# Kernel tuning notes

Measured on AMD Instinct MI355X. Metric: run time of the kernel, lower is better.

Reference implementation:

```python
import jax, jax.numpy as jnp
import numpy as np

N_NODES = 80000


def gcn_conv(x, W, b, src, dst, n_nodes):
    """PyG GCNConv: add self-loops, symmetric normalization, linear, scatter-add, bias."""
    h = x @ W  # [N, out]
    loop = jnp.arange(n_nodes, dtype=src.dtype)
    s = jnp.concatenate([src, loop])  # [E+N]
    d = jnp.concatenate([dst, loop])
    deg = jax.ops.segment_sum(jnp.ones_like(d, dtype=h.dtype), d, num_segments=n_nodes)
    dinv = jnp.where(deg > 0, jax.lax.rsqrt(deg), 0.0)  # deg^-0.5, inf->0
    norm = dinv[s] * dinv[d]  # [E+N]
    msg = h[s] * norm[:, None]  # gather + scale
    out = jax.ops.segment_sum(msg, d, num_segments=n_nodes)  # scatter-add at dst
    return out + b


def setup_inputs() -> dict:
    key = jax.random.key(0)
    ks = jax.random.split(key, 8)
    n_in, n_hid, n_out = 64, 64, 32
    n_edges = 1280000
    x = jax.random.normal(ks[0], (N_NODES, n_in), dtype=jnp.float32)
    edge_index = jax.random.randint(ks[1], (2, n_edges), 0, N_NODES, dtype=jnp.int64)
    def glorot(k, fan_in, fan_out):
        lim = np.sqrt(6.0 / (fan_in + fan_out))
        return jax.random.uniform(k, (fan_in, fan_out), jnp.float32, -lim, lim)
    return {
        "x": x,
        "W1": glorot(ks[2], n_in, n_hid), "b1": jnp.zeros((n_hid,), jnp.float32),
        "W2": glorot(ks[3], n_hid, n_hid), "b2": jnp.zeros((n_hid,), jnp.float32),
        "W3": glorot(ks[4], n_hid, n_out), "b3": jnp.zeros((n_out,), jnp.float32),
        "edge_index": edge_index,
    }


def reference(x, W1, b1, W2, b2, W3, b3, edge_index):
    src, dst = edge_index[0], edge_index[1]
    n = x.shape[0]
    # eval mode: dropout(p=0.2) is identity
    h = jax.nn.elu(gcn_conv(x, W1, b1, src, dst, n))
    h = jax.nn.elu(gcn_conv(h, W2, b2, src, dst, n))
    return gcn_conv(h, W3, b3, src, dst, n)
```

## Files before the change

kernel.cpp:

```cpp
#include <hip/hip_runtime.h>
#include <cmath>


__global__ __launch_bounds__(256) void k_hist_gemm1(
    const int* __restrict__ dst, int nE, int nN,
    int* __restrict__ cnt4, int* __restrict__ rankp,
    const float* __restrict__ x, const float* __restrict__ W,
    float* __restrict__ h, int n) {
    constexpr int OUT = 64;
    constexpr int CG = OUT / 4;
    constexpr int RG = 256 / CG;
    constexpr int ROWS = RG * 4;
    constexpr int XLD = 68;
    __shared__ float Ws[64 * OUT];
    __shared__ float xs[ROWS * XLD];

    const int tid = threadIdx.x;

    if (blockIdx.x & 1) {
        const int bid = blockIdx.x >> 1;
        const int t = bid * 256 + tid;
        const int e0 = t * 4;
        const int sh = (tid >> 6) & 3;
        int* __restrict__ mycnt = cnt4 + (size_t)sh * nN;
        if (e0 + 4 <= nE) {
            int4 d = *reinterpret_cast<const int4*>(dst + e0);
            int r0 = atomicAdd(&mycnt[d.x], 1);
            int r1 = atomicAdd(&mycnt[d.y], 1);
            int r2 = atomicAdd(&mycnt[d.z], 1);
            int r3 = atomicAdd(&mycnt[d.w], 1);
            *reinterpret_cast<int4*>(rankp + e0) =
                make_int4(r0 | (sh << 28), r1 | (sh << 28),
                          r2 | (sh << 28), r3 | (sh << 28));
        } else {
            for (int e = e0; e < nE; ++e)
                rankp[e] = atomicAdd(&mycnt[dst[e]], 1) | (sh << 28);
        }
        return;
    }

    const int bid = blockIdx.x >> 1;
    const int row0 = bid * ROWS;

#pragma unroll
    for (int i = tid * 4; i < 64 * OUT; i += 1024)
        *reinterpret_cast<float4*>(&Ws[i]) =
            *reinterpret_cast<const float4*>(&W[i]);

#pragma unroll
    for (int it = 0; it < ROWS / 16; ++it) {
        const int flat = it * 1024 + tid * 4;
        const int r = flat >> 6;
        const int k = flat & 63;
        float4 v;
        if (row0 + r < n)
            v = *reinterpret_cast<const float4*>(x + (size_t)(row0 + r) * 64 + k);
        else
            v = make_float4(0.f, 0.f, 0.f, 0.f);
        *reinterpret_cast<float4*>(&xs[r * XLD + k]) = v;
    }
    __syncthreads();

    const int rg = tid / CG;
    const int cg = tid % CG;
    const int r0 = rg * 4;

    float4 acc[4];
#pragma unroll
    for (int i = 0; i < 4; ++i) acc[i] = make_float4(0.f, 0.f, 0.f, 0.f);

#pragma unroll 2
    for (int kc = 0; kc < 16; ++kc) {
        float4 xr[4], wk[4];
#pragma unroll
        for (int i = 0; i < 4; ++i)
            xr[i] = *reinterpret_cast<const float4*>(&xs[(r0 + i) * XLD + kc * 4]);
#pragma unroll
        for (int kk = 0; kk < 4; ++kk)
            wk[kk] = *reinterpret_cast<const float4*>(&Ws[(kc * 4 + kk) * OUT + cg * 4]);
#pragma unroll
        for (int kk = 0; kk < 4; ++kk) {
#pragma unroll
            for (int i = 0; i < 4; ++i) {
                const float xv = (kk == 0) ? xr[i].x
                               : (kk == 1) ? xr[i].y
                               : (kk == 2) ? xr[i].z
                                           : xr[i].w;
                acc[i].x += xv * wk[kk].x;
                acc[i].y += xv * wk[kk].y;
                acc[i].z += xv * wk[kk].z;
                acc[i].w += xv * wk[kk].w;
            }
        }
    }

#pragma unroll
    for (int i = 0; i < 4; ++i) {
        const int row = row0 + r0 + i;
        if (row < n)
            *reinterpret_cast<float4*>(h + (size_t)row * OUT + cg * 4) = acc[i];
    }
}

__global__ __launch_bounds__(256) void k_scan1(const int* __restrict__ cnt4, int n,
                                               int* __restrict__ bsum) {
    __shared__ int s[256];
    int i = blockIdx.x * 256 + threadIdx.x;
    int v = 0;
    if (i < n)
        v = cnt4[i] + cnt4[n + i] + cnt4[2 * n + i] + cnt4[3 * n + i];
    s[threadIdx.x] = v;
    __syncthreads();
    for (int off = 128; off > 0; off >>= 1) {
        if (threadIdx.x < off) s[threadIdx.x] += s[threadIdx.x + off];
        __syncthreads();
    }
    if (threadIdx.x == 0) bsum[blockIdx.x] = s[0];
}

__global__ __launch_bounds__(256) void k_scan3(const int* __restrict__ cnt4, int n,
                                               const int* __restrict__ bsum,
                                               int* __restrict__ row_start,
                                               int4* __restrict__ base4,
                                               float* __restrict__ dinv) {
    __shared__ int red[256];
    __shared__ int s[256];
    const int bid = blockIdx.x;
    int part = 0;
    for (int i = threadIdx.x; i < bid; i += 256) part += bsum[i];
    red[threadIdx.x] = part;
    __syncthreads();
    for (int off = 128; off > 0; off >>= 1) {
        if (threadIdx.x < off) red[threadIdx.x] += red[threadIdx.x + off];
        __syncthreads();
    }
    const int boff = red[0];

    int i = bid * 256 + threadIdx.x;
    int c0 = 0, c1 = 0, c2 = 0, c3 = 0;
    if (i < n) {
        c0 = cnt4[i];
        c1 = cnt4[n + i];
        c2 = cnt4[2 * n + i];
        c3 = cnt4[3 * n + i];
    }
    const int v = c0 + c1 + c2 + c3;
    s[threadIdx.x] = v;
    __syncthreads();
    for (int off = 1; off < 256; off <<= 1) {
        int t = (threadIdx.x >= off) ? s[threadIdx.x - off] : 0;
        __syncthreads();
        s[threadIdx.x] += t;
        __syncthreads();
    }
    if (i < n) {
        const int ex = boff + s[threadIdx.x] - v;
        row_start[i] = ex;
        base4[i] = make_int4(ex, ex + c0, ex + c0 + c1, ex + c0 + c1 + c2);
        dinv[i] = rsqrtf((float)v + 1.0f);
        if (i == n - 1) row_start[n] = ex + v;
    }
}

__global__ __launch_bounds__(256) void k_fill_csr(
    const int* __restrict__ src, const int* __restrict__ dst,
    const int* __restrict__ rankp, const int4* __restrict__ base4,
    int nE, int* __restrict__ csr) {
    const int t = blockIdx.x * 256 + threadIdx.x;
    const int e0 = t * 4;
    if (e0 + 4 <= nE) {
        int4 d = *reinterpret_cast<const int4*>(dst + e0);
        int4 s = *reinterpret_cast<const int4*>(src + e0);
        int4 rp = *reinterpret_cast<const int4*>(rankp + e0);
        int4 b0 = base4[d.x];
        int4 b1 = base4[d.y];
        int4 b2 = base4[d.z];
        int4 b3 = base4[d.w];
        auto pick = [](const int4& b, int sh) {
            return sh == 0 ? b.x : sh == 1 ? b.y : sh == 2 ? b.z : b.w;
        };
        csr[pick(b0, rp.x >> 28) + (rp.x & 0x0FFFFFFF)] = s.x;
        csr[pick(b1, rp.y >> 28) + (rp.y & 0x0FFFFFFF)] = s.y;
        csr[pick(b2, rp.z >> 28) + (rp.z & 0x0FFFFFFF)] = s.z;
        csr[pick(b3, rp.w >> 28) + (rp.w & 0x0FFFFFFF)] = s.w;
    } else {
        for (int e = e0; e < nE; ++e) {
            int rp = rankp[e];
            int4 b = base4[dst[e]];
            int sh = rp >> 28;
            int base = sh == 0 ? b.x : sh == 1 ? b.y : sh == 2 ? b.z : b.w;
            csr[base + (rp & 0x0FFFFFFF)] = src[e];
        }
    }
}

template <bool SCALE_SRC, int OUTW>
__global__ __launch_bounds__(256) void k_agg_gemm(
    const float* __restrict__ g, const int* __restrict__ row_start,
    const int* __restrict__ csr, const float* __restrict__ dinv,
    const float* __restrict__ b, const float* __restrict__ W,
    float* __restrict__ gout, int n) {
    constexpr int TPN = 16, NPB = 16;
    __shared__ float Ws[64 * OUTW];
    __shared__ float hs[NPB][68];

    const int tid = threadIdx.x;
#pragma unroll
    for (int i = tid * 4; i < 64 * OUTW; i += 1024)
        *reinterpret_cast<float4*>(&Ws[i]) =
            *reinterpret_cast<const float4*>(&W[i]);

    const int node = blockIdx.x * NPB + tid / TPN;
    const int sub = tid % TPN;
    const bool valid = node < n;

    float4 o = make_float4(0.f, 0.f, 0.f, 0.f);
    float dv = 0.f;
    if (valid) {
        const int r0 = row_start[node];
        const int r1 = row_start[node + 1];
        dv = dinv[node];
        float4 acc = *reinterpret_cast<const float4*>(g + (size_t)node * 64 + sub * 4);
        if (SCALE_SRC) { acc.x *= dv; acc.y *= dv; acc.z *= dv; acc.w *= dv; }
        int j = r0;
        for (; j + 4 <= r1; j += 4) {
            int s0 = csr[j], s1 = csr[j + 1], s2 = csr[j + 2], s3 = csr[j + 3];
            float4 v0 = *reinterpret_cast<const float4*>(g + (size_t)s0 * 64 + sub * 4);
            float4 v1 = *reinterpret_cast<const float4*>(g + (size_t)s1 * 64 + sub * 4);
            float4 v2 = *reinterpret_cast<const float4*>(g + (size_t)s2 * 64 + sub * 4);
            float4 v3 = *reinterpret_cast<const float4*>(g + (size_t)s3 * 64 + sub * 4);
            if (SCALE_SRC) {
                float w0 = dinv[s0], w1 = dinv[s1], w2 = dinv[s2], w3 = dinv[s3];
                acc.x += w0 * v0.x + w1 * v1.x + w2 * v2.x + w3 * v3.x;
                acc.y += w0 * v0.y + w1 * v1.y + w2 * v2.y + w3 * v3.y;
                acc.z += w0 * v0.z + w1 * v1.z + w2 * v2.z + w3 * v3.z;
                acc.w += w0 * v0.w + w1 * v1.w + w2 * v2.w + w3 * v3.w;
            } else {
                acc.x += v0.x + v1.x + v2.x + v3.x;
                acc.y += v0.y + v1.y + v2.y + v3.y;
                acc.z += v0.z + v1.z + v2.z + v3.z;
                acc.w += v0.w + v1.w + v2.w + v3.w;
            }
        }
        for (; j < r1; ++j) {
            int s = csr[j];
            float4 v = *reinterpret_cast<const float4*>(g + (size_t)s * 64 + sub * 4);
            float w = SCALE_SRC ? dinv[s] : 1.0f;
            acc.x += w * v.x; acc.y += w * v.y; acc.z += w * v.z; acc.w += w * v.w;
        }
        const float4 bb = *reinterpret_cast<const float4*>(b + sub * 4);
        o.x = dv * acc.x + bb.x;
        o.y = dv * acc.y + bb.y;
        o.z = dv * acc.z + bb.z;
        o.w = dv * acc.w + bb.w;
        o.x = o.x > 0.f ? o.x : expm1f(o.x);
        o.y = o.y > 0.f ? o.y : expm1f(o.y);
        o.z = o.z > 0.f ? o.z : expm1f(o.z);
        o.w = o.w > 0.f ? o.w : expm1f(o.w);
    }
    *reinterpret_cast<float4*>(&hs[tid / TPN][sub * 4]) = o;
    __syncthreads();

    constexpr int CG2 = OUTW / 4;
    if (tid < NPB * CG2) {
        const int n2 = tid / CG2;
        const int cg2 = tid % CG2;
        float4 a2 = make_float4(0.f, 0.f, 0.f, 0.f);
#pragma unroll
        for (int k4 = 0; k4 < 16; ++k4) {
            float4 h4 = *reinterpret_cast<const float4*>(&hs[n2][k4 * 4]);
            float4 w0 = *reinterpret_cast<const float4*>(&Ws[(k4 * 4 + 0) * OUTW + cg2 * 4]);
            float4 w1 = *reinterpret_cast<const float4*>(&Ws[(k4 * 4 + 1) * OUTW + cg2 * 4]);
            float4 w2 = *reinterpret_cast<const float4*>(&Ws[(k4 * 4 + 2) * OUTW + cg2 * 4]);
            float4 w3 = *reinterpret_cast<const float4*>(&Ws[(k4 * 4 + 3) * OUTW + cg2 * 4]);
            a2.x += h4.x * w0.x + h4.y * w1.x + h4.z * w2.x + h4.w * w3.x;
            a2.y += h4.x * w0.y + h4.y * w1.y + h4.z * w2.y + h4.w * w3.y;
            a2.z += h4.x * w0.z + h4.y * w1.z + h4.z * w2.z + h4.w * w3.z;
            a2.w += h4.x * w0.w + h4.y * w1.w + h4.z * w2.w + h4.w * w3.w;
        }
        const int gn = blockIdx.x * NPB + n2;
        if (gn < n) {
            const float dv2 = dinv[gn];
            a2.x *= dv2; a2.y *= dv2; a2.z *= dv2; a2.w *= dv2;
            *reinterpret_cast<float4*>(gout + (size_t)gn * OUTW + cg2 * 4) = a2;
        }
    }
}

template <int FEAT, bool ELU>
__global__ __launch_bounds__(256) void k_aggregate(
    const float* __restrict__ g, const int* __restrict__ row_start,
    const int* __restrict__ csr, const float* __restrict__ dinv,
    const float* __restrict__ b, float* __restrict__ out, int n) {
    constexpr int TPN = FEAT / 4;
    constexpr int NPB = 256 / TPN;
    const int tid = threadIdx.x;
    const int node = blockIdx.x * NPB + tid / TPN;
    const int sub = tid % TPN;
    if (node >= n) return;

    const int r0 = row_start[node];
    const int r1 = row_start[node + 1];
    float4 acc = *reinterpret_cast<const float4*>(g + (size_t)node * FEAT + sub * 4);

    int j = r0;
    for (; j + 4 <= r1; j += 4) {
        int s0 = csr[j], s1 = csr[j + 1], s2 = csr[j + 2], s3 = csr[j + 3];
        float4 v0 = *reinterpret_cast<const float4*>(g + (size_t)s0 * FEAT + sub * 4);
        float4 v1 = *reinterpret_cast<const float4*>(g + (size_t)s1 * FEAT + sub * 4);
        float4 v2 = *reinterpret_cast<const float4*>(g + (size_t)s2 * FEAT + sub * 4);
        float4 v3 = *reinterpret_cast<const float4*>(g + (size_t)s3 * FEAT + sub * 4);
        acc.x += v0.x + v1.x + v2.x + v3.x;
        acc.y += v0.y + v1.y + v2.y + v3.y;
        acc.z += v0.z + v1.z + v2.z + v3.z;
        acc.w += v0.w + v1.w + v2.w + v3.w;
    }
    for (; j < r1; ++j) {
        int s = csr[j];
        float4 v = *reinterpret_cast<const float4*>(g + (size_t)s * FEAT + sub * 4);
        acc.x += v.x; acc.y += v.y; acc.z += v.z; acc.w += v.w;
    }

    const float dv = dinv[node];
    const float4 bb = *reinterpret_cast<const float4*>(b + sub * 4);
    float4 o;
    o.x = dv * acc.x + bb.x;
    o.y = dv * acc.y + bb.y;
    o.z = dv * acc.z + bb.z;
    o.w = dv * acc.w + bb.w;
    if (ELU) {
        o.x = o.x > 0.f ? o.x : expm1f(o.x);
        o.y = o.y > 0.f ? o.y : expm1f(o.y);
        o.z = o.z > 0.f ? o.z : expm1f(o.z);
        o.w = o.w > 0.f ? o.w : expm1f(o.w);
    }
    *reinterpret_cast<float4*>(out + (size_t)node * FEAT + sub * 4) = o;
}

extern "C" void kernel_launch(void* const* d_in, const int* in_sizes, int n_in,
                              void* d_out, int out_size, void* d_ws, size_t ws_size,
                              hipStream_t stream) {
    const float* x  = (const float*)d_in[0];
    const float* W1 = (const float*)d_in[1];
    const float* b1 = (const float*)d_in[2];
    const float* W2 = (const float*)d_in[3];
    const float* b2 = (const float*)d_in[4];
    const float* W3 = (const float*)d_in[5];
    const float* b3 = (const float*)d_in[6];
    const int*   ei = (const int*)d_in[7];

    const int N  = in_sizes[0] / 64;
    const int E  = in_sizes[7] / 2;
    const int* src = ei;
    const int* dst = ei + E;

    auto cdiv = [](long long a, long long b) { return (int)((a + b - 1) / b); };
    const int NB = cdiv(N, 256);

    float* ws = (float*)d_ws;
    float* dinv = ws;
    float* A    = dinv + N;
    float* C    = A + (size_t)N * 64;
    int* cnt4      = (int*)(C + (size_t)N * 64);
    int4* base4    = (int4*)(cnt4 + 4 * (size_t)N);
    int* row_start = (int*)(base4 + N);
    int* csr       = row_start + N + 1;
    int* bsum      = csr + E;
    int* rankp     = (int*)C;
    float* out = (float*)d_out;

    hipMemsetAsync(cnt4, 0, sizeof(int) * 4 * (size_t)N, stream);
    const int histBlocks = cdiv(E, 1024);
    const int gemmBlocks = cdiv(N, 64);
    k_hist_gemm1<<<histBlocks + gemmBlocks, 256, 0, stream>>>(
        dst, E, N, cnt4, rankp, x, W1, A, N);
    k_scan1<<<NB, 256, 0, stream>>>(cnt4, N, bsum);
    k_scan3<<<NB, 256, 0, stream>>>(cnt4, N, bsum, row_start, base4, dinv);
    k_fill_csr<<<cdiv(E, 1024), 256, 0, stream>>>(src, dst, rankp, base4, E, csr);

    k_agg_gemm<true, 64><<<cdiv(N, 16), 256, 0, stream>>>(
        A, row_start, csr, dinv, b1, W2, C, N);

    k_agg_gemm<false, 32><<<cdiv(N, 16), 256, 0, stream>>>(
        C, row_start, csr, dinv, b2, W3, A, N);

    k_aggregate<32, false><<<cdiv(N, 32), 256, 0, stream>>>(
        A, row_start, csr, dinv, b3, out, N);
}
```

Before: 292.6 us.

## Store intermediate node features in fp16 to halve gather traffic

The hidden feature buffers (the GEMM1 output and both aggregate+GEMM outputs) are now written as packed half2 values instead of fp32, while accumulation stays in fp32. The aggregation kernels are adjusted to match: each thread loads eight halves per neighbour with one 16-byte load, so fewer threads serve each node and more nodes fit in a block. This is meant to cut the memory bandwidth spent on the irregular neighbour gathers, which dominate runtime. In exchange it adds fp16 rounding error to the intermediate activations, which could push results past the accuracy tolerance.

```diff
diff --git a/kernel.cpp b/kernel.cpp
--- a/kernel.cpp
+++ b/kernel.cpp
@@ -1,4 +1,5 @@
 #include <hip/hip_runtime.h>
+#include <hip/hip_fp16.h>
 #include <cmath>
 
 
@@ -6,7 +7,7 @@
     const int* __restrict__ dst, int nE, int nN,
     int* __restrict__ cnt4, int* __restrict__ rankp,
     const float* __restrict__ x, const float* __restrict__ W,
-    float* __restrict__ h, int n) {
+    __half* __restrict__ h, int n) {
     constexpr int OUT = 64;
     constexpr int CG = OUT / 4;
     constexpr int RG = 256 / CG;
@@ -97,8 +98,13 @@
 #pragma unroll
     for (int i = 0; i < 4; ++i) {
         const int row = row0 + r0 + i;
-        if (row < n)
-            *reinterpret_cast<float4*>(h + (size_t)row * OUT + cg * 4) = acc[i];
+        if (row < n) {
+            __half2 p0 = __floats2half2_rn(acc[i].x, acc[i].y);
+            __half2 p1 = __floats2half2_rn(acc[i].z, acc[i].w);
+            uint2 u = make_uint2(*reinterpret_cast<unsigned int*>(&p0),
+                                 *reinterpret_cast<unsigned int*>(&p1));
+            *reinterpret_cast<uint2*>(h + (size_t)row * 64 + cg * 4) = u;
+        }
     }
 }
 
@@ -194,13 +200,23 @@
     }
 }
 
+__device__ __forceinline__ void add_half8(float* a, const uint4& raw, float w) {
+    const __half2* hp = reinterpret_cast<const __half2*>(&raw);
+#pragma unroll
+    for (int q = 0; q < 4; ++q) {
+        float2 f = __half22float2(hp[q]);
+        a[q * 2 + 0] += w * f.x;
+        a[q * 2 + 1] += w * f.y;
+    }
+}
+
 template <bool SCALE_SRC, int OUTW>
 __global__ __launch_bounds__(256) void k_agg_gemm(
-    const float* __restrict__ g, const int* __restrict__ row_start,
+    const __half* __restrict__ g, const int* __restrict__ row_start,
     const int* __restrict__ csr, const float* __restrict__ dinv,
     const float* __restrict__ b, const float* __restrict__ W,
-    float* __restrict__ gout, int n) {
-    constexpr int TPN = 16, NPB = 16;
+    __half* __restrict__ gout, int n) {
+    constexpr int TPN = 8, NPB = 32;
     __shared__ float Ws[64 * OUTW];
     __shared__ float hs[NPB][68];
 
@@ -210,61 +226,65 @@
         *reinterpret_cast<float4*>(&Ws[i]) =
             *reinterpret_cast<const float4*>(&W[i]);
 
-    const int node = blockIdx.x * NPB + tid / TPN;
+    const int nloc = tid / TPN;
     const int sub = tid % TPN;
+    const int node = blockIdx.x * NPB + nloc;
     const bool valid = node < n;
 
-    float4 o = make_float4(0.f, 0.f, 0.f, 0.f);
+    float a[8];
+#pragma unroll
+    for (int q = 0; q < 8; ++q) a[q] = 0.f;
     float dv = 0.f;
+
     if (valid) {
         const int r0 = row_start[node];
         const int r1 = row_start[node + 1];
         dv = dinv[node];
-        float4 acc = *reinterpret_cast<const float4*>(g + (size_t)node * 64 + sub * 4);
-        if (SCALE_SRC) { acc.x *= dv; acc.y *= dv; acc.z *= dv; acc.w *= dv; }
+        {
+            uint4 raw = *reinterpret_cast<const uint4*>(g + (size_t)node * 64 + sub * 8);
+            add_half8(a, raw, SCALE_SRC ? dv : 1.0f);
+        }
         int j = r0;
         for (; j + 4 <= r1; j += 4) {
             int s0 = csr[j], s1 = csr[j + 1], s2 = csr[j + 2], s3 = csr[j + 3];
-            float4 v0 = *reinterpret_cast<const float4*>(g + (size_t)s0 * 64 + sub * 4);
-            float4 v1 = *reinterpret_cast<const float4*>(g + (size_t)s1 * 64 + sub * 4);
-            float4 v2 = *reinterpret_cast<const float4*>(g + (size_t)s2 * 64 + sub * 4);
-            float4 v3 = *reinterpret_cast<const float4*>(g + (size_t)s3 * 64 + sub * 4);
+            uint4 v0 = *reinterpret_cast<const uint4*>(g + (size_t)s0 * 64 + sub * 8);
+            uint4 v1 = *reinterpret_cast<const uint4*>(g + (size_t)s1 * 64 + sub * 8);
+            uint4 v2 = *reinterpret_cast<const uint4*>(g + (size_t)s2 * 64 + sub * 8);
+            uint4 v3 = *reinterpret_cast<const uint4*>(g + (size_t)s3 * 64 + sub * 8);
             if (SCALE_SRC) {
-                float w0 = dinv[s0], w1 = dinv[s1], w2 = dinv[s2], w3 = dinv[s3];
-                acc.x += w0 * v0.x + w1 * v1.x + w2 * v2.x + w3 * v3.x;
-                acc.y += w0 * v0.y + w1 * v1.y + w2 * v2.y + w3 * v3.y;
-                acc.z += w0 * v0.z + w1 * v1.z + w2 * v2.z + w3 * v3.z;
-                acc.w += w0 * v0.w + w1 * v1.w + w2 * v2.w + w3 * v3.w;
+                add_half8(a, v0, dinv[s0]);
+                add_half8(a, v1, dinv[s1]);
+                add_half8(a, v2, dinv[s2]);
+                add_half8(a, v3, dinv[s3]);
             } else {
-                acc.x += v0.x + v1.x + v2.x + v3.x;
-                acc.y += v0.y + v1.y + v2.y + v3.y;
-                acc.z += v0.z + v1.z + v2.z + v3.z;
-                acc.w += v0.w + v1.w + v2.w + v3.w;
+                add_half8(a, v0, 1.0f);
+                add_half8(a, v1, 1.0f);
+                add_half8(a, v2, 1.0f);
+                add_half8(a, v3, 1.0f);
             }
         }
         for (; j < r1; ++j) {
             int s = csr[j];
-            float4 v = *reinterpret_cast<const float4*>(g + (size_t)s * 64 + sub * 4);
-            float w = SCALE_SRC ? dinv[s] : 1.0f;
-            acc.x += w * v.x; acc.y += w * v.y; acc.z += w * v.z; acc.w += w * v.w;
-        }
-        const float4 bb = *reinterpret_cast<const float4*>(b + sub * 4);
-        o.x = dv * acc.x + bb.x;
-        o.y = dv * acc.y + bb.y;
-        o.z = dv * acc.z + bb.z;
-        o.w = dv * acc.w + bb.w;
-        o.x = o.x > 0.f ? o.x : expm1f(o.x);
-        o.y = o.y > 0.f ? o.y : expm1f(o.y);
-        o.z = o.z > 0.f ? o.z : expm1f(o.z);
-        o.w = o.w > 0.f ? o.w : expm1f(o.w);
-    }
-    *reinterpret_cast<float4*>(&hs[tid / TPN][sub * 4]) = o;
+            uint4 v = *reinterpret_cast<const uint4*>(g + (size_t)s * 64 + sub * 8);
+            add_half8(a, v, SCALE_SRC ? dinv[s] : 1.0f);
+        }
+        float4 bb0 = *reinterpret_cast<const float4*>(b + sub * 8);
+        float4 bb1 = *reinterpret_cast<const float4*>(b + sub * 8 + 4);
+#pragma unroll
+        for (int q = 0; q < 8; ++q) {
+            float o = dv * a[q] + ((q < 4) ? (&bb0.x)[q] : (&bb1.x)[q - 4]);
+            o = o > 0.f ? o : expm1f(o);
+            a[q] = o;
+        }
+    }
+    *reinterpret_cast<float4*>(&hs[nloc][sub * 8]) = make_float4(a[0], a[1], a[2], a[3]);
+    *reinterpret_cast<float4*>(&hs[nloc][sub * 8 + 4]) = make_float4(a[4], a[5], a[6], a[7]);
     __syncthreads();
 
     constexpr int CG2 = OUTW / 4;
-    if (tid < NPB * CG2) {
-        const int n2 = tid / CG2;
-        const int cg2 = tid % CG2;
+    for (int t2 = tid; t2 < NPB * CG2; t2 += 256) {
+        const int n2 = t2 / CG2;
+        const int cg2 = t2 % CG2;
         float4 a2 = make_float4(0.f, 0.f, 0.f, 0.f);
 #pragma unroll
         for (int k4 = 0; k4 < 16; ++k4) {
@@ -281,19 +301,20 @@
         const int gn = blockIdx.x * NPB + n2;
         if (gn < n) {
             const float dv2 = dinv[gn];
-            a2.x *= dv2; a2.y *= dv2; a2.z *= dv2; a2.w *= dv2;
-            *reinterpret_cast<float4*>(gout + (size_t)gn * OUTW + cg2 * 4) = a2;
-        }
-    }
-}
-
-template <int FEAT, bool ELU>
-__global__ __launch_bounds__(256) void k_aggregate(
-    const float* __restrict__ g, const int* __restrict__ row_start,
+            __half2 p0 = __floats2half2_rn(a2.x * dv2, a2.y * dv2);
+            __half2 p1 = __floats2half2_rn(a2.z * dv2, a2.w * dv2);
+            uint2 u = make_uint2(*reinterpret_cast<unsigned int*>(&p0),
+                                 *reinterpret_cast<unsigned int*>(&p1));
+            *reinterpret_cast<uint2*>(gout + (size_t)gn * OUTW + cg2 * 4) = u;
+        }
+    }
+}
+
+__global__ __launch_bounds__(256) void k_aggregate3(
+    const __half* __restrict__ g, const int* __restrict__ row_start,
     const int* __restrict__ csr, const float* __restrict__ dinv,
     const float* __restrict__ b, float* __restrict__ out, int n) {
-    constexpr int TPN = FEAT / 4;
-    constexpr int NPB = 256 / TPN;
+    constexpr int TPN = 4, NPB = 64;
     const int tid = threadIdx.x;
     const int node = blockIdx.x * NPB + tid / TPN;
     const int sub = tid % TPN;
@@ -301,40 +322,45 @@
 
     const int r0 = row_start[node];
     const int r1 = row_start[node + 1];
-    float4 acc = *reinterpret_cast<const float4*>(g + (size_t)node * FEAT + sub * 4);
-
+    float a[8];
+#pragma unroll
+    for (int q = 0; q < 8; ++q) a[q] = 0.f;
+    {
+        uint4 raw = *reinterpret_cast<const uint4*>(g + (size_t)node * 32 + sub * 8);
+        add_half8(a, raw, 1.0f);
+    }
     int j = r0;
     for (; j + 4 <= r1; j += 4) {
         int s0 = csr[j], s1 = csr[j + 1], s2 = csr[j + 2], s3 = csr[j + 3];
-        float4 v0 = *reinterpret_cast<const float4*>(g + (size_t)s0 * FEAT + sub * 4);
-        float4 v1 = *reinterpret_cast<const float4*>(g + (size_t)s1 * FEAT + sub * 4);
-        float4 v2 = *reinterpret_cast<const float4*>(g + (size_t)s2 * FEAT + sub * 4);
-        float4 v3 = *reinterpret_cast<const float4*>(g + (size_t)s3 * FEAT + sub * 4);
-        acc.x += v0.x + v1.x + v2.x + v3.x;
-        acc.y += v0.y + v1.y + v2.y + v3.y;
-        acc.z += v0.z + v1.z + v2.z + v3.z;
-        acc.w += v0.w + v1.w + v2.w + v3.w;
+        uint4 v0 = *reinterpret_cast<const uint4*>(g + (size_t)s0 * 32 + sub * 8);
+        uint4 v1 = *reinterpret_cast<const uint4*>(g + (size_t)s1 * 32 + sub * 8);
+        uint4 v2 = *reinterpret_cast<const uint4*>(g + (size_t)s2 * 32 + sub * 8);
+        uint4 v3 = *reinterpret_cast<const uint4*>(g + (size_t)s3 * 32 + sub * 8);
+        add_half8(a, v0, 1.0f);
+        add_half8(a, v1, 1.0f);
+        add_half8(a, v2, 1.0f);
+        add_half8(a, v3, 1.0f);
     }
     for (; j < r1; ++j) {
         int s = csr[j];
-        float4 v = *reinterpret_cast<const float4*>(g + (size_t)s * FEAT + sub * 4);
-        acc.x += v.x; acc.y += v.y; acc.z += v.z; acc.w += v.w;
+        uint4 v = *reinterpret_cast<const uint4*>(g + (size_t)s * 32 + sub * 8);
+        add_half8(a, v, 1.0f);
     }
 
     const float dv = dinv[node];
-    const float4 bb = *reinterpret_cast<const float4*>(b + sub * 4);
-    float4 o;
-    o.x = dv * acc.x + bb.x;
-    o.y = dv * acc.y + bb.y;
-    o.z = dv * acc.z + bb.z;
-    o.w = dv * acc.w + bb.w;
-    if (ELU) {
-        o.x = o.x > 0.f ? o.x : expm1f(o.x);
-        o.y = o.y > 0.f ? o.y : expm1f(o.y);
-        o.z = o.z > 0.f ? o.z : expm1f(o.z);
-        o.w = o.w > 0.f ? o.w : expm1f(o.w);
-    }
-    *reinterpret_cast<float4*>(out + (size_t)node * FEAT + sub * 4) = o;
+    float4 bb0 = *reinterpret_cast<const float4*>(b + sub * 8);
+    float4 bb1 = *reinterpret_cast<const float4*>(b + sub * 8 + 4);
+    float4 o0, o1;
+    o0.x = dv * a[0] + bb0.x;
+    o0.y = dv * a[1] + bb0.y;
+    o0.z = dv * a[2] + bb0.z;
+    o0.w = dv * a[3] + bb0.w;
+    o1.x = dv * a[4] + bb1.x;
+    o1.y = dv * a[5] + bb1.y;
+    o1.z = dv * a[6] + bb1.z;
+    o1.w = dv * a[7] + bb1.w;
+    *reinterpret_cast<float4*>(out + (size_t)node * 32 + sub * 8) = o0;
+    *reinterpret_cast<float4*>(out + (size_t)node * 32 + sub * 8 + 4) = o1;
 }
 
 extern "C" void kernel_launch(void* const* d_in, const int* in_sizes, int n_in,
@@ -359,9 +385,9 @@
 
     float* ws = (float*)d_ws;
     float* dinv = ws;
-    float* A    = dinv + N;
-    float* C    = A + (size_t)N * 64;
-    int* cnt4      = (int*)(C + (size_t)N * 64);
+    __half* A   = (__half*)(dinv + N);
+    __half* C   = (__half*)(dinv + N + (size_t)N * 32);
+    int* cnt4      = (int*)(dinv + N + (size_t)N * 64);
     int4* base4    = (int4*)(cnt4 + 4 * (size_t)N);
     int* row_start = (int*)(base4 + N);
     int* csr       = row_start + N + 1;
@@ -378,12 +404,12 @@
     k_scan3<<<NB, 256, 0, stream>>>(cnt4, N, bsum, row_start, base4, dinv);
     k_fill_csr<<<cdiv(E, 1024), 256, 0, stream>>>(src, dst, rankp, base4, E, csr);
 
-    k_agg_gemm<true, 64><<<cdiv(N, 16), 256, 0, stream>>>(
+    k_agg_gemm<true, 64><<<cdiv(N, 32), 256, 0, stream>>>(
         A, row_start, csr, dinv, b1, W2, C, N);
 
-    k_agg_gemm<false, 32><<<cdiv(N, 16), 256, 0, stream>>>(
-        C, row_start, csr, dinv, b2, W3, A, N);
-
-    k_aggregate<32, false><<<cdiv(N, 32), 256, 0, stream>>>(
-        A, row_start, csr, dinv, b3, out, N);
-}
+    k_agg_gemm<false, 32><<<cdiv(N, 32), 256, 0, stream>>>(
+        C, row_start, csr, dinv, b2, W3, (__half*)A, N);
+
+    k_aggregate3<<<cdiv(N, 64), 256, 0, stream>>>(
+        (__half*)A, row_start, csr, dinv, b3, out, N);
+}
```

After: 247.2 us. -15.5%, faster.
